# Performance work log

Measured on AMD Instinct MI355X. Metric: run time of the kernel, lower is better.

## Reference

```python
import jax, jax.numpy as jnp
import numpy as np

N, E = 10000, 160000
RNA, PROT, EMB, HID, H = 2000, 100, 128, 128, 4
D_IN = 2 * EMB          # 256, input to last block
D_MID = HID * 4         # 512, after conv1/lin1 residual (heads*channel)


def _gat(x, src, dst, Ws, Wd, att_s, att_d, bias, n_nodes, heads):
    # PyG GATConv (tuple in_channels -> separate src/dst linears, concat=True,
    # add_self_loops=False, negative_slope=0.2, eval mode so dropout is identity)
    C = Ws.shape[1] // heads
    xs = (x @ Ws).reshape(n_nodes, heads, C)   # [N,H,C]
    xd = (x @ Wd).reshape(n_nodes, heads, C)
    a_s = jnp.sum(xs * att_s, axis=-1)          # [N,H]
    a_d = jnp.sum(xd * att_d, axis=-1)
    alpha = jax.nn.leaky_relu(a_s[src] + a_d[dst], 0.2)   # [E,H]
    m = jax.ops.segment_max(alpha, dst, num_segments=n_nodes)  # [N,H]
    alpha = jnp.exp(alpha - m[dst])
    denom = jax.ops.segment_sum(alpha, dst, num_segments=n_nodes)
    alpha = alpha / (denom[dst] + 1e-16)
    out = jax.ops.segment_sum(xs[src] * alpha[:, :, None], dst, num_segments=n_nodes)
    return out.reshape(n_nodes, heads * C) + bias


def _layernorm(h, g, b, eps=1e-5):
    mu = jnp.mean(h, axis=-1, keepdims=True)
    var = jnp.mean(jnp.square(h - mu), axis=-1, keepdims=True)
    return (h - mu) * jax.lax.rsqrt(var + eps) * g + b


def setup_inputs() -> dict:
    key = jax.random.key(0)
    ks = iter(jax.random.split(key, 40))
    w = lambda *s: jax.random.normal(next(ks), s, jnp.float32) * 0.02
    z = lambda *s: jnp.zeros(s, jnp.float32)
    inp = {}
    inp["x"] = jax.random.normal(next(ks), (N, RNA + PROT), jnp.float32)
    inp["edge_index"] = jax.random.randint(next(ks), (2, E), 0, N, jnp.int64)
    inp["W_rna"], inp["b_rna"] = w(RNA, EMB), z(EMB)
    inp["W_prot"], inp["b_prot"] = w(PROT, EMB), z(EMB)
    # last GraphAttnBlock (hidden_dim -> hidden_dim), the only one whose output is used
    inp["c1_Ws"], inp["c1_Wd"] = w(D_IN, H * HID), w(D_IN, H * HID)
    inp["c1_as"], inp["c1_ad"] = w(H, HID), w(H, HID)
    inp["c1_b"] = z(H * HID)
    inp["l1_W"], inp["l1_b"] = w(D_IN, D_MID), z(D_MID)
    inp["ln_g"], inp["ln_b"] = jnp.ones((D_MID,), jnp.float32), z(D_MID)
    inp["c2_Ws"], inp["c2_Wd"] = w(D_MID, H * HID), w(D_MID, H * HID)
    inp["c2_as"], inp["c2_ad"] = w(H, HID), w(H, HID)
    inp["c2_b"] = z(H * HID)
    inp["l2_W"], inp["l2_b"] = w(D_MID, D_MID), z(D_MID)
    inp["agg_W"], inp["agg_b"] = w(D_MID, HID), z(HID)
    inp["dr_W"], inp["dr_b"] = w(HID, EMB), z(EMB)
    inp["dp_W"], inp["dp_b"] = w(HID, EMB), z(EMB)
    inp["rr_W"], inp["rr_b"] = w(EMB, RNA), z(RNA)
    inp["rp_W"], inp["rp_b"] = w(EMB, PROT), z(PROT)
    return inp


def reference(x, edge_index, W_rna, b_rna, W_prot, b_prot,
              c1_Ws, c1_Wd, c1_as, c1_ad, c1_b, l1_W, l1_b, ln_g, ln_b,
              c2_Ws, c2_Wd, c2_as, c2_ad, c2_b, l2_W, l2_b,
              agg_W, agg_b, dr_W, dr_b, dp_W, dp_b, rr_W, rr_b, rp_W, rp_b):
    src, dst = edge_index[0], edge_index[1]
    rna_e = x[:, :RNA] @ W_rna + b_rna
    prot_e = x[:, RNA:] @ W_prot + b_prot
    xin = jnp.concatenate([rna_e, prot_e], axis=1)   # raw_x_input [N, 2*EMB]
    # source loops blocks over raw_x_input; only last block output survives
    h = _gat(xin, src, dst, c1_Ws, c1_Wd, c1_as, c1_ad, c1_b, N, H) + (xin @ l1_W + l1_b)
    h = jax.nn.relu(_layernorm(h, ln_g, ln_b))
    h = _gat(h, src, dst, c2_Ws, c2_Wd, c2_as, c2_ad, c2_b, N, H) + (h @ l2_W + l2_b)
    emb = jax.nn.relu(h @ agg_W + agg_b)
    rna_recon = (emb @ dr_W + dr_b) @ rr_W + rr_b
    prot_recon = (emb @ dp_W + dp_b) @ rp_W + rp_b
    return (rna_recon, prot_recon, emb)
```

## Files before the change

kernel.cpp:

```cpp
#include <hip/hip_runtime.h>
#include <hip/hip_bf16.h>
#include <stdint.h>
#include <stddef.h>

using bf16  = __hip_bfloat16;
using bf162 = __hip_bfloat162;

typedef __bf16 bvec8 __attribute__((ext_vector_type(8)));
typedef float  fvec4 __attribute__((ext_vector_type(4)));

struct __align__(16) bf16x8 { bf162 a, b, c, d; };

__device__ __forceinline__ void bf8_to_f(const bf16* p, float* o) {
    bf16x8 v = *reinterpret_cast<const bf16x8*>(p);
    o[0] = __bfloat162float(v.a.x); o[1] = __bfloat162float(v.a.y);
    o[2] = __bfloat162float(v.b.x); o[3] = __bfloat162float(v.b.y);
    o[4] = __bfloat162float(v.c.x); o[5] = __bfloat162float(v.c.y);
    o[6] = __bfloat162float(v.d.x); o[7] = __bfloat162float(v.d.y);
}

__device__ __forceinline__ float wred_sum(float v) {
    #pragma unroll
    for (int o = 32; o > 0; o >>= 1) v += __shfl_xor(v, o);
    return v;
}

__device__ __forceinline__ float wred_max(float v) {
    #pragma unroll
    for (int o = 32; o > 0; o >>= 1) v = fmaxf(v, __shfl_xor(v, o));
    return v;
}

__device__ __forceinline__ float lrelu(float x) { return (x > 0.f) ? x : 0.2f * x; }

__device__ __forceinline__ fvec4 mfma16(bvec8 a, bvec8 b, fvec4 c) {
    return __builtin_amdgcn_mfma_f32_16x16x32_bf16(a, b, c, 0, 0, 0);
}

__device__ __forceinline__ bvec8 ldA(const bf16* p) {
    return *reinterpret_cast<const bvec8*>(p);
}
__device__ __forceinline__ bvec8 ldA(const float* p) {
    float4 f0 = *reinterpret_cast<const float4*>(p);
    float4 f1 = *reinterpret_cast<const float4*>(p + 4);
    union { bvec8 v; bf16 h[8]; } u;
    u.h[0] = __float2bfloat16(f0.x); u.h[1] = __float2bfloat16(f0.y);
    u.h[2] = __float2bfloat16(f0.z); u.h[3] = __float2bfloat16(f0.w);
    u.h[4] = __float2bfloat16(f1.x); u.h[5] = __float2bfloat16(f1.y);
    u.h[6] = __float2bfloat16(f1.z); u.h[7] = __float2bfloat16(f1.w);
    return u.v;
}

__global__ void detect_kernel(const int* __restrict__ ei, int E, int* __restrict__ flags) {
    __shared__ int zc;
    if (threadIdx.x == 0) zc = 0;
    __syncthreads();
    int nodd = E / 2; if (nodd > 1024) nodd = 1024;
    for (int i = threadIdx.x; i < nodd; i += blockDim.x)
        if (ei[2 * i + 1] == 0) atomicAdd(&zc, 1);
    __syncthreads();
    if (threadIdx.x == 0) flags[0] = (zc > nodd / 2) ? 1 : 0;
}

__global__ void conv_edges_kernel(const int* __restrict__ ei, int* __restrict__ src32,
                                  int* __restrict__ dst32, int E, int N,
                                  const int* __restrict__ flags) {
    const int e = blockIdx.x * blockDim.x + threadIdx.x;
    if (e >= E) return;
    int s, d;
    if (flags[0]) { s = ei[2 * e]; d = ei[2 * (E + e)]; }
    else          { s = ei[e];     d = ei[E + e]; }
    src32[e] = (s < 0) ? 0 : ((s >= N) ? N - 1 : s);
    dst32[e] = (d < 0) ? 0 : ((d >= N) ? N - 1 : d);
}

__global__ void zero2_kernel(int* __restrict__ p1, int* __restrict__ p2, int n) {
    int i = blockIdx.x * blockDim.x + threadIdx.x;
    if (i < n) { p1[i] = 0; p2[i] = 0; }
}

__global__ void hist_kernel(const int* __restrict__ dst32, int* __restrict__ cnt, int E) {
    int e = blockIdx.x * blockDim.x + threadIdx.x;
    if (e < E) atomicAdd(&cnt[dst32[e]], 1);
}

__global__ __launch_bounds__(1024) void scan_kernel(const int* __restrict__ cnt,
                                                    int* __restrict__ row_ptr, int N) {
    __shared__ int wsum[16];
    __shared__ int carry;
    const int tid = threadIdx.x, lane = tid & 63, wid = tid >> 6;
    if (tid == 0) { carry = 0; row_ptr[0] = 0; }
    __syncthreads();
    for (int base = 0; base < N; base += 1024) {
        int i = base + tid;
        int v = (i < N) ? cnt[i] : 0;
        int s = v;
        #pragma unroll
        for (int o = 1; o < 64; o <<= 1) {
            int t = __shfl_up(s, o);
            if (lane >= o) s += t;
        }
        if (lane == 63) wsum[wid] = s;
        __syncthreads();
        if (wid == 0 && lane < 16) {
            int ws = wsum[lane];
            #pragma unroll
            for (int o = 1; o < 16; o <<= 1) {
                int t = __shfl_up(ws, o);
                if (lane >= o) ws += t;
            }
            wsum[lane] = ws;
        }
        __syncthreads();
        int add = carry + (wid > 0 ? wsum[wid - 1] : 0);
        if (i < N) row_ptr[i + 1] = s + add;
        __syncthreads();
        if (tid == 0) carry += wsum[15];
        __syncthreads();
    }
}

__global__ void fill_csr_kernel(const int* __restrict__ src32, const int* __restrict__ dst32,
                                const int* __restrict__ row_ptr, int* __restrict__ cursor,
                                int* __restrict__ col_src, int E) {
    int e = blockIdx.x * blockDim.x + threadIdx.x;
    if (e >= E) return;
    int d = dst32[e];
    int pos = atomicAdd(&cursor[d], 1);
    col_src[row_ptr[d] + pos] = src32[e];
}

struct TEnt { const float* src; bf16* dst; int K, N, Kp, Np, tstart; };
struct TTab { TEnt e[12]; int n; };

__global__ __launch_bounds__(256) void wconv_t_kernel(TTab tab) {
    __shared__ float tile[32][33];
    const int b = blockIdx.x;
    int wi = 0;
    #pragma unroll 1
    for (int i = 1; i < tab.n; ++i) if (b >= tab.e[i].tstart) wi = i;
    const TEnt w = tab.e[wi];
    const int tidx = b - w.tstart;
    const int ntk = w.Kp >> 5;
    const int tn = tidx / ntk, tk = tidx - tn * ntk;
    const int k0 = tk * 32, n0 = tn * 32;
    const int tx = threadIdx.x & 31, ty = threadIdx.x >> 5;
    #pragma unroll
    for (int j = 0; j < 4; ++j) {
        int k = k0 + ty * 4 + j;
        int n = n0 + tx;
        tile[ty * 4 + j][tx] = (k < w.K && n < w.N) ? w.src[(size_t)k * w.N + n] : 0.f;
    }
    __syncthreads();
    #pragma unroll
    for (int j = 0; j < 4; ++j) {
        int n = n0 + ty * 4 + j;
        int k = k0 + tx;
        w.dst[(size_t)n * w.Kp + k] = __float2bfloat16(tile[tx][ty * 4 + j]);
    }
}

__global__ __launch_bounds__(256) void conv_x_kernel(const float* __restrict__ x,
                                                     bf16* __restrict__ xbf) {
    const int r = blockIdx.x;
    const float* xr = x + (size_t)r * 2100;
    bf16* orow = xbf + (size_t)r * 2128;
    #pragma unroll
    for (int pass = 0; pass < 2; ++pass) {
        int c0 = pass * 2048 + threadIdx.x * 8;
        if (c0 >= 2128) continue;
        union { uint4 u; bf16 h[8]; } ob;
        if (c0 + 8 <= 2100) {
            float4 f0 = *reinterpret_cast<const float4*>(xr + c0);
            float4 f1 = *reinterpret_cast<const float4*>(xr + c0 + 4);
            ob.h[0] = __float2bfloat16(f0.x); ob.h[1] = __float2bfloat16(f0.y);
            ob.h[2] = __float2bfloat16(f0.z); ob.h[3] = __float2bfloat16(f0.w);
            ob.h[4] = __float2bfloat16(f1.x); ob.h[5] = __float2bfloat16(f1.y);
            ob.h[6] = __float2bfloat16(f1.z); ob.h[7] = __float2bfloat16(f1.w);
        } else {
            #pragma unroll
            for (int j = 0; j < 8; ++j) {
                int c = c0 + j;
                ob.h[j] = __float2bfloat16((c < 2100) ? xr[c] : 0.f);
            }
        }
        *reinterpret_cast<uint4*>(orow + c0) = ob.u;
    }
}

__global__ void bias_fuse_kernel(const float* l1_b, const float* c1_b, float* bsum1,
                                 const float* l2_b, const float* c2_b, float* bsum2,
                                 const float* dr_b, const float* dp_b, float* ddb) {
    int i = blockIdx.x * blockDim.x + threadIdx.x;
    if (i < 512)       bsum1[i] = l1_b[i] + c1_b[i];
    else if (i < 1024) bsum2[i - 512] = l2_b[i - 512] + c2_b[i - 512];
    else if (i < 1152) ddb[i - 1024] = dr_b[i - 1024];
    else if (i < 1280) ddb[i - 1024] = dp_b[i - 1152];
}

__global__ __launch_bounds__(64) void logits_bf16_kernel(
    const bf16* __restrict__ X,
    const float* __restrict__ Vs, const float* __restrict__ Vd,
    float* __restrict__ a_s, float* __restrict__ a_d)
{
    const int n = blockIdx.x, lane = threadIdx.x;
    const int c0 = lane * 4;
    union { uint2 u; bf16 h[4]; } ub;
    ub.u = *reinterpret_cast<const uint2*>(X + (size_t)n * 256 + c0);
    const float vv[4] = {__bfloat162float(ub.h[0]), __bfloat162float(ub.h[1]),
                         __bfloat162float(ub.h[2]), __bfloat162float(ub.h[3])};
    float ss0=0,ss1=0,ss2=0,ss3=0, dd0=0,dd1=0,dd2=0,dd3=0;
    #pragma unroll
    for (int j = 0; j < 4; ++j) {
        float4 vs = *reinterpret_cast<const float4*>(Vs + (size_t)(c0 + j) * 4);
        float4 vd = *reinterpret_cast<const float4*>(Vd + (size_t)(c0 + j) * 4);
        ss0 = fmaf(vv[j], vs.x, ss0); ss1 = fmaf(vv[j], vs.y, ss1);
        ss2 = fmaf(vv[j], vs.z, ss2); ss3 = fmaf(vv[j], vs.w, ss3);
        dd0 = fmaf(vv[j], vd.x, dd0); dd1 = fmaf(vv[j], vd.y, dd1);
        dd2 = fmaf(vv[j], vd.z, dd2); dd3 = fmaf(vv[j], vd.w, dd3);
    }
    ss0 = wred_sum(ss0); ss1 = wred_sum(ss1); ss2 = wred_sum(ss2); ss3 = wred_sum(ss3);
    dd0 = wred_sum(dd0); dd1 = wred_sum(dd1); dd2 = wred_sum(dd2); dd3 = wred_sum(dd3);
    if (lane == 0) {
        a_s[n*4+0]=ss0; a_s[n*4+1]=ss1; a_s[n*4+2]=ss2; a_s[n*4+3]=ss3;
        a_d[n*4+0]=dd0; a_d[n*4+1]=dd1; a_d[n*4+2]=dd2; a_d[n*4+3]=dd3;
    }
}

template <int FM, bool RELU, typename AT>
__global__ __launch_bounds__(256) void mfma_gemm_kernel(
    const AT* __restrict__ A, int lda,
    const bf16* __restrict__ Bt, int ldb,
    const float* __restrict__ bias,
    float* __restrict__ Cf, int ldcf,
    bf16* __restrict__ Cb, int ldcb,
    int M, int Nn, int K)
{
    const int tid  = threadIdx.x;
    const int w    = tid >> 6, lane = tid & 63;
    const int wr   = w >> 1,   wc   = w & 1;
    const int m0   = blockIdx.y * (FM * 32) + wr * (FM * 16);
    const int n0   = blockIdx.x * 64 + wc * 32;
    const int lrow = lane & 15;
    const int lk8  = (lane >> 4) * 8;

    const AT* Ap[FM];
    #pragma unroll
    for (int i = 0; i < FM; ++i) {
        int r = m0 + i * 16 + lrow;
        if (r > M - 1) r = M - 1;
        Ap[i] = A + (size_t)r * lda + lk8;
    }
    const bf16* Bp = Bt + (size_t)(n0 + lrow) * ldb + lk8;
    const size_t b16 = (size_t)16 * ldb;

    fvec4 acc[FM][2];
    const fvec4 z = {0.f, 0.f, 0.f, 0.f};
    #pragma unroll
    for (int i = 0; i < FM; ++i) { acc[i][0] = z; acc[i][1] = z; }

    #pragma unroll 2
    for (int k = 0; k < K; k += 32) {
        bvec8 b0 = *reinterpret_cast<const bvec8*>(Bp + k);
        bvec8 b1 = *reinterpret_cast<const bvec8*>(Bp + k + b16);
        #pragma unroll
        for (int i = 0; i < FM; ++i) {
            bvec8 a = ldA(Ap[i] + k);
            acc[i][0] = mfma16(a, b0, acc[i][0]);
            acc[i][1] = mfma16(a, b1, acc[i][1]);
        }
    }

    const int r4 = (lane >> 4) * 4;
    #pragma unroll
    for (int fn = 0; fn < 2; ++fn) {
        const int col = n0 + fn * 16 + lrow;
        if (col >= Nn) continue;
        const float bz = bias ? bias[col] : 0.f;
        #pragma unroll
        for (int fm = 0; fm < FM; ++fm) {
            const int rbase = m0 + fm * 16 + r4;
            #pragma unroll
            for (int r = 0; r < 4; ++r) {
                const int row = rbase + r;
                if (row >= M) continue;
                float v = acc[fm][fn][r] + bz;
                if (RELU) v = fmaxf(v, 0.f);
                if (Cf) Cf[(size_t)row * ldcf + col] = v;
                if (Cb) Cb[(size_t)row * ldcb + col] = __float2bfloat16(v);
            }
        }
    }
}

__global__ __launch_bounds__(256) void mfma_gemm_dual_kernel(
    const bf16* __restrict__ A, int lda,
    const bf16* __restrict__ Bt, int ldb,
    const float* __restrict__ biasU,
    bf16* __restrict__ xs, float* __restrict__ hB,
    int M, int K)
{
    const int tid  = threadIdx.x;
    const int w    = tid >> 6, lane = tid & 63;
    const int wr   = w >> 1,   wc   = w & 1;
    const int m0   = blockIdx.y * 128 + wr * 64;
    const int n0   = blockIdx.x * 128 + wc * 64;
    const int lrow = lane & 15;
    const int lk8  = (lane >> 4) * 8;

    const bf16* Ap[4];
    const bf16* Bp[4];
    #pragma unroll
    for (int i = 0; i < 4; ++i) {
        int r = m0 + i * 16 + lrow;
        if (r > M - 1) r = M - 1;
        Ap[i] = A + (size_t)r * lda + lk8;
        Bp[i] = Bt + (size_t)(n0 + i * 16 + lrow) * ldb + lk8;
    }

    fvec4 acc[4][4];
    const fvec4 z = {0.f, 0.f, 0.f, 0.f};
    #pragma unroll
    for (int i = 0; i < 4; ++i)
        #pragma unroll
        for (int j = 0; j < 4; ++j) acc[i][j] = z;

    #pragma unroll 2
    for (int k = 0; k < K; k += 32) {
        bvec8 a[4], b[4];
        #pragma unroll
        for (int i = 0; i < 4; ++i) a[i] = *reinterpret_cast<const bvec8*>(Ap[i] + k);
        #pragma unroll
        for (int j = 0; j < 4; ++j) b[j] = *reinterpret_cast<const bvec8*>(Bp[j] + k);
        #pragma unroll
        for (int i = 0; i < 4; ++i)
            #pragma unroll
            for (int j = 0; j < 4; ++j)
                acc[i][j] = mfma16(a[i], b[j], acc[i][j]);
    }

    const int r4 = (lane >> 4) * 4;
    #pragma unroll
    for (int fn = 0; fn < 4; ++fn) {
        const int col = n0 + fn * 16 + lrow;
        if (col < 512) {
            #pragma unroll
            for (int fm = 0; fm < 4; ++fm) {
                const int rbase = m0 + fm * 16 + r4;
                #pragma unroll
                for (int r = 0; r < 4; ++r) {
                    const int row = rbase + r;
                    if (row >= M) continue;
                    xs[(size_t)row * 512 + col] = __float2bfloat16(acc[fm][fn][r]);
                }
            }
        } else {
            const int c2 = col - 512;
            const float bz = biasU[c2];
            #pragma unroll
            for (int fm = 0; fm < 4; ++fm) {
                const int rbase = m0 + fm * 16 + r4;
                #pragma unroll
                for (int r = 0; r < 4; ++r) {
                    const int row = rbase + r;
                    if (row >= M) continue;
                    hB[(size_t)row * 512 + c2] = acc[fm][fn][r] + bz;
                }
            }
        }
    }
}

__global__ void make_v2_kernel(const float* __restrict__ Ws, const float* __restrict__ atts,
                               float* __restrict__ Vs,
                               const float* __restrict__ Wd, const float* __restrict__ attd,
                               float* __restrict__ Vd, int K)
{
    int t = blockIdx.x * blockDim.x + threadIdx.x;
    const int half = K * 4;
    if (t >= 2 * half) return;
    const float* W   = (t < half) ? Ws : Wd;
    const float* att = (t < half) ? atts : attd;
    float* V         = (t < half) ? Vs : Vd;
    int tt = (t < half) ? t : t - half;
    int k = tt >> 2, h = tt & 3;
    float s = 0.f;
    const float* wp = W + (size_t)k * 512 + h * 128;
    const float* ap = att + h * 128;
    #pragma unroll 4
    for (int c = 0; c < 128; ++c)
        s = fmaf(wp[c], ap[c], s);
    V[k * 4 + h] = s;
}

__global__ __launch_bounds__(64) void gat_gather_kernel(
    const int* __restrict__ row_ptr, const int* __restrict__ col_src,
    const float* __restrict__ a_s, const float* __restrict__ a_d,
    const bf16* __restrict__ xs, float* __restrict__ hout,
    bf16* __restrict__ hout_bf)
{
    const int d = blockIdx.x, lane = threadIdx.x;
    const int beg = row_ptr[d], end = row_ptr[d + 1];
    const float4 ad = *reinterpret_cast<const float4*>(a_d + (size_t)d * 4);

    float m0=-1e30f, m1=-1e30f, m2=-1e30f, m3=-1e30f;
    for (int i = beg + lane; i < end; i += 64) {
        int s = col_src[i];
        float4 as = *reinterpret_cast<const float4*>(a_s + (size_t)s * 4);
        m0 = fmaxf(m0, lrelu(as.x + ad.x));
        m1 = fmaxf(m1, lrelu(as.y + ad.y));
        m2 = fmaxf(m2, lrelu(as.z + ad.z));
        m3 = fmaxf(m3, lrelu(as.w + ad.w));
    }
    m0 = wred_max(m0); m1 = wred_max(m1); m2 = wred_max(m2); m3 = wred_max(m3);

    float d0=0.f, d1=0.f, d2=0.f, d3=0.f;
    for (int i = beg + lane; i < end; i += 64) {
        int s = col_src[i];
        float4 as = *reinterpret_cast<const float4*>(a_s + (size_t)s * 4);
        d0 += __expf(lrelu(as.x + ad.x) - m0);
        d1 += __expf(lrelu(as.y + ad.y) - m1);
        d2 += __expf(lrelu(as.z + ad.z) - m2);
        d3 += __expf(lrelu(as.w + ad.w) - m3);
    }
    d0 = wred_sum(d0); d1 = wred_sum(d1); d2 = wred_sum(d2); d3 = wred_sum(d3);

    const int h = lane >> 4;
    const float mh   = (h == 0) ? m0 : ((h == 1) ? m1 : ((h == 2) ? m2 : m3));
    const float adh  = (h == 0) ? ad.x : ((h == 1) ? ad.y : ((h == 2) ? ad.z : ad.w));
    const float den  = (h == 0) ? d0 : ((h == 1) ? d1 : ((h == 2) ? d2 : d3));
    const float invd = 1.0f / (den + 1e-16f);
    const int c0 = lane * 8;
    float acc[8] = {0.f,0.f,0.f,0.f,0.f,0.f,0.f,0.f};
    #pragma unroll 2
    for (int i = beg; i < end; ++i) {
        int s = col_src[i];
        float coef = __expf(lrelu(a_s[(size_t)s * 4 + h] + adh) - mh) * invd;
        float xv[8];
        bf8_to_f(xs + (size_t)s * 512 + c0, xv);
        #pragma unroll
        for (int t = 0; t < 8; ++t) acc[t] = fmaf(coef, xv[t], acc[t]);
    }
    float* hp = hout + (size_t)d * 512 + c0;
    if (hout_bf) {
        bf16* hb = hout_bf + (size_t)d * 512 + c0;
        #pragma unroll
        for (int t = 0; t < 8; ++t) {
            float fv = hp[t] + acc[t];
            hp[t] = fv;
            hb[t] = __float2bfloat16(fv);
        }
    } else {
        #pragma unroll
        for (int t = 0; t < 8; ++t) hp[t] += acc[t];
    }
}

__global__ __launch_bounds__(64) void ln_relu_logits_kernel(
    const float* __restrict__ in, const float* __restrict__ g,
    const float* __restrict__ b,
    const float* __restrict__ Vs, const float* __restrict__ Vd,
    bf16* __restrict__ outbf, float* __restrict__ a_s, float* __restrict__ a_d)
{
    const int n = blockIdx.x, lane = threadIdx.x;
    const int c0 = lane * 8;
    const float* ip = in + (size_t)n * 512 + c0;
    float v[8];
    float4 p0 = *reinterpret_cast<const float4*>(ip);
    float4 p1 = *reinterpret_cast<const float4*>(ip + 4);
    v[0]=p0.x; v[1]=p0.y; v[2]=p0.z; v[3]=p0.w; v[4]=p1.x; v[5]=p1.y; v[6]=p1.z; v[7]=p1.w;
    float s = 0.f;
    #pragma unroll
    for (int t = 0; t < 8; ++t) s += v[t];
    s = wred_sum(s);
    const float mu = s * (1.0f / 512.0f);
    float q = 0.f;
    #pragma unroll
    for (int t = 0; t < 8; ++t) { float dlt = v[t] - mu; q = fmaf(dlt, dlt, q); }
    q = wred_sum(q);
    const float sc = rsqrtf(q * (1.0f / 512.0f) + 1e-5f);
    float4 g0 = *reinterpret_cast<const float4*>(g + c0);
    float4 g1 = *reinterpret_cast<const float4*>(g + c0 + 4);
    float4 b0 = *reinterpret_cast<const float4*>(b + c0);
    float4 b1 = *reinterpret_cast<const float4*>(b + c0 + 4);
    const float gv[8] = {g0.x,g0.y,g0.z,g0.w,g1.x,g1.y,g1.z,g1.w};
    const float bv[8] = {b0.x,b0.y,b0.z,b0.w,b1.x,b1.y,b1.z,b1.w};
    float r[8];
    bf16* ob = outbf + (size_t)n * 512 + c0;
    #pragma unroll
    for (int t = 0; t < 8; ++t) {
        r[t] = fmaxf(0.f, fmaf((v[t] - mu) * sc, gv[t], bv[t]));
        ob[t] = __float2bfloat16(r[t]);
    }
    float ss0=0,ss1=0,ss2=0,ss3=0, dd0=0,dd1=0,dd2=0,dd3=0;
    #pragma unroll
    for (int t = 0; t < 8; ++t) {
        float4 vs = *reinterpret_cast<const float4*>(Vs + (size_t)(c0 + t) * 4);
        float4 vd = *reinterpret_cast<const float4*>(Vd + (size_t)(c0 + t) * 4);
        ss0 = fmaf(r[t], vs.x, ss0); ss1 = fmaf(r[t], vs.y, ss1);
        ss2 = fmaf(r[t], vs.z, ss2); ss3 = fmaf(r[t], vs.w, ss3);
        dd0 = fmaf(r[t], vd.x, dd0); dd1 = fmaf(r[t], vd.y, dd1);
        dd2 = fmaf(r[t], vd.z, dd2); dd3 = fmaf(r[t], vd.w, dd3);
    }
    ss0 = wred_sum(ss0); ss1 = wred_sum(ss1); ss2 = wred_sum(ss2); ss3 = wred_sum(ss3);
    dd0 = wred_sum(dd0); dd1 = wred_sum(dd1); dd2 = wred_sum(dd2); dd3 = wred_sum(dd3);
    if (lane == 0) {
        a_s[n*4+0]=ss0; a_s[n*4+1]=ss1; a_s[n*4+2]=ss2; a_s[n*4+3]=ss3;
        a_d[n*4+0]=dd0; a_d[n*4+1]=dd1; a_d[n*4+2]=dd2; a_d[n*4+3]=dd3;
    }
}

extern "C" void kernel_launch(void* const* d_in, const int* in_sizes, int n_in,
                              void* d_out, int out_size, void* d_ws, size_t ws_size,
                              hipStream_t stream)
{
    (void)n_in; (void)out_size; (void)ws_size;
    const float* x   = (const float*)d_in[0];
    const int*   ei  = (const int*)d_in[1];

    const float* W_rna  = (const float*)d_in[2];
    const float* b_rna  = (const float*)d_in[3];
    const float* W_prot = (const float*)d_in[4];
    const float* b_prot = (const float*)d_in[5];
    const float* c1_Ws  = (const float*)d_in[6];
    const float* c1_Wd  = (const float*)d_in[7];
    const float* c1_as  = (const float*)d_in[8];
    const float* c1_ad  = (const float*)d_in[9];
    const float* c1_b   = (const float*)d_in[10];
    const float* l1_W   = (const float*)d_in[11];
    const float* l1_b   = (const float*)d_in[12];
    const float* ln_g   = (const float*)d_in[13];
    const float* ln_b   = (const float*)d_in[14];
    const float* c2_Ws  = (const float*)d_in[15];
    const float* c2_Wd  = (const float*)d_in[16];
    const float* c2_as  = (const float*)d_in[17];
    const float* c2_ad  = (const float*)d_in[18];
    const float* c2_b   = (const float*)d_in[19];
    const float* l2_W   = (const float*)d_in[20];
    const float* l2_b   = (const float*)d_in[21];
    const float* agg_W  = (const float*)d_in[22];
    const float* agg_b  = (const float*)d_in[23];
    const float* dr_W   = (const float*)d_in[24];
    const float* dr_b   = (const float*)d_in[25];
    const float* dp_W   = (const float*)d_in[26];
    const float* dp_b   = (const float*)d_in[27];
    const float* rr_W   = (const float*)d_in[28];
    const float* rr_b   = (const float*)d_in[29];
    const float* rp_W   = (const float*)d_in[30];
    const float* rp_b   = (const float*)d_in[31];

    const int N = in_sizes[0] / 2100;
    const int E = in_sizes[1] / 2;
    const int Mp = ((N + 127) & ~127) + 128;

    char* wsp = (char*)d_ws;
    size_t off = 0;
    auto alloc = [&](size_t bytes) -> void* {
        void* p = wsp + off;
        off += (bytes + 255) & ~(size_t)255;
        return p;
    };
    int*      flags   = (int*)   alloc(16);
    int*      src32   = (int*)   alloc((size_t)E * 4);
    int*      dst32   = (int*)   alloc((size_t)E * 4);
    int*      cnt     = (int*)   alloc((size_t)N * 4);
    int*      cursor  = (int*)   alloc((size_t)N * 4);
    int*      row_ptr = (int*)   alloc((size_t)(N + 1) * 4);
    int*      col_src = (int*)   alloc((size_t)E * 4);
    float*    hB      = (float*) alloc((size_t)N * 512 * 4);
    float*    a_s     = (float*) alloc((size_t)N * 4 * 4);
    float*    a_d     = (float*) alloc((size_t)N * 4 * 4);
    float*    Vs      = (float*) alloc(512 * 4 * 4);
    float*    Vd      = (float*) alloc(512 * 4 * 4);
    float*    bsum1   = (float*) alloc(512 * 4);
    float*    bsum2   = (float*) alloc(512 * 4);
    float*    ddb     = (float*) alloc(256 * 4);
    bf16*     xbf     = (bf16*)  alloc((size_t)Mp * 2128 * 2);
    bf16*     xin_bf  = (bf16*)  alloc((size_t)Mp * 256 * 2);
    bf16*     hA_bf   = (bf16*)  alloc((size_t)Mp * 512 * 2);
    bf16*     hB_bf   = (bf16*)  alloc((size_t)Mp * 512 * 2);
    bf16*     xs      = (bf16*)  alloc((size_t)Mp * 512 * 2);
    bf16*     emb_bf  = (bf16*)  alloc((size_t)Mp * 128 * 2);
    bf16*     trp     = (bf16*)  alloc((size_t)Mp * 256 * 2);
    bf16*     wrna_t  = (bf16*)  alloc((size_t)128 * 2016 * 2);
    bf16*     wprot_t = (bf16*)  alloc((size_t)128 * 128 * 2);
    bf16*     cb1     = (bf16*)  alloc((size_t)1024 * 256 * 2);
    bf16*     cb2     = (bf16*)  alloc((size_t)1024 * 512 * 2);
    bf16*     aggt    = (bf16*)  alloc((size_t)128 * 512 * 2);
    bf16*     ddt     = (bf16*)  alloc((size_t)256 * 128 * 2);
    bf16*     rrt     = (bf16*)  alloc((size_t)2048 * 128 * 2);
    bf16*     rpt     = (bf16*)  alloc((size_t)128 * 128 * 2);

    const dim3 blk64(64, 1, 1);
    const dim3 blk256(256, 1, 1);
    const dim3 gE((E + 255) / 256);
    const dim3 gN((N + 255) / 256);
    const int GY128 = (N + 127) / 128;
    const int GY64  = (N + 63) / 64;
    const int GY32  = (N + 31) / 32;

    float* out0 = (float*)d_out;
    float* out1 = out0 + (size_t)N * 2000;
    float* out2 = out1 + (size_t)N * 100;

    detect_kernel<<<dim3(1), blk256, 0, stream>>>(ei, E, flags);
    conv_edges_kernel<<<gE, blk256, 0, stream>>>(ei, src32, dst32, E, N, flags);
    zero2_kernel<<<gN, blk256, 0, stream>>>(cnt, cursor, N);
    hist_kernel<<<gE, blk256, 0, stream>>>(dst32, cnt, E);
    scan_kernel<<<dim3(1), dim3(1024, 1, 1), 0, stream>>>(cnt, row_ptr, N);
    fill_csr_kernel<<<gE, blk256, 0, stream>>>(src32, dst32, row_ptr, cursor, col_src, E);

    {
        TTab tab{};
        int nt = 0, i = 0;
        auto add = [&](const float* s, bf16* d, int K, int Nn, int Kp, int Np) {
            tab.e[i] = {s, d, K, Nn, Kp, Np, nt};
            nt += (Kp >> 5) * (Np >> 5);
            ++i;
        };
        add(W_rna,  wrna_t,          2000, 128, 2016, 128);
        add(W_prot, wprot_t,          100, 128,  128, 128);
        add(c1_Ws,  cb1,              256, 512,  256, 512);
        add(l1_W,   cb1 + 512 * 256,  256, 512,  256, 512);
        add(c2_Ws,  cb2,              512, 512,  512, 512);
        add(l2_W,   cb2 + 512 * 512,  512, 512,  512, 512);
        add(agg_W,  aggt,             512, 128,  512, 128);
        add(dr_W,   ddt,              128, 128,  128, 128);
        add(dp_W,   ddt + 128 * 128,  128, 128,  128, 128);
        add(rr_W,   rrt,              128, 2000, 128, 2048);
        add(rp_W,   rpt,              128, 100,  128, 128);
        tab.n = i;
        wconv_t_kernel<<<dim3(nt), blk256, 0, stream>>>(tab);
    }
    bias_fuse_kernel<<<dim3(5), blk256, 0, stream>>>(l1_b, c1_b, bsum1,
                                                     l2_b, c2_b, bsum2,
                                                     dr_b, dp_b, ddb);
    make_v2_kernel<<<dim3((2 * 256 * 4 + 255) / 256), blk256, 0, stream>>>(
        c1_Ws, c1_as, Vs, c1_Wd, c1_ad, Vd, 256);

    conv_x_kernel<<<dim3(N), blk256, 0, stream>>>(x, xbf);
    mfma_gemm_kernel<2, false, bf16><<<dim3(2, GY64), blk256, 0, stream>>>(
        xbf, 2128, wrna_t, 2016, b_rna, nullptr, 0, xin_bf, 256, N, 128, 2016);
    mfma_gemm_kernel<1, false, bf16><<<dim3(2, GY32), blk256, 0, stream>>>(
        xbf + 2000, 2128, wprot_t, 128, b_prot, nullptr, 0, xin_bf + 128, 256, N, 128, 128);
    logits_bf16_kernel<<<dim3(N), blk64, 0, stream>>>(xin_bf, Vs, Vd, a_s, a_d);

    mfma_gemm_dual_kernel<<<dim3(8, GY128), blk256, 0, stream>>>(
        xin_bf, 256, cb1, 256, bsum1, xs, hB, N, 256);
    gat_gather_kernel<<<dim3(N), blk64, 0, stream>>>(row_ptr, col_src, a_s, a_d, xs, hB, nullptr);

    make_v2_kernel<<<dim3((2 * 512 * 4 + 255) / 256), blk256, 0, stream>>>(
        c2_Ws, c2_as, Vs, c2_Wd, c2_ad, Vd, 512);
    ln_relu_logits_kernel<<<dim3(N), blk64, 0, stream>>>(
        hB, ln_g, ln_b, Vs, Vd, hA_bf, a_s, a_d);

    mfma_gemm_dual_kernel<<<dim3(8, GY128), blk256, 0, stream>>>(
        hA_bf, 512, cb2, 512, bsum2, xs, hB, N, 512);
    gat_gather_kernel<<<dim3(N), blk64, 0, stream>>>(row_ptr, col_src, a_s, a_d, xs, hB, hB_bf);

    mfma_gemm_kernel<2, true, bf16><<<dim3(2, GY64), blk256, 0, stream>>>(
        hB_bf, 512, aggt, 512, agg_b, out2, 128, emb_bf, 128, N, 128, 512);
    mfma_gemm_kernel<2, false, bf16><<<dim3(4, GY64), blk256, 0, stream>>>(
        emb_bf, 128, ddt, 128, ddb, nullptr, 0, trp, 256, N, 256, 128);
    mfma_gemm_kernel<4, false, bf16><<<dim3(32, GY128), blk256, 0, stream>>>(
        trp, 256, rrt, 128, rr_b, out0, 2000, nullptr, 0, N, 2000, 128);
    mfma_gemm_kernel<2, false, bf16><<<dim3(2, GY64), blk256, 0, stream>>>(
        trp + 128, 256, rpt, 128, rp_b, out1, 100, nullptr, 0, N, 100, 128);
}
```

Baseline: 584.7 us.

## Widen dual GEMM tiles to 128x256 with 512 threads and XCD-aware block remap

The dual GEMM (source projection plus linear residual) now uses 512-thread blocks with 8 waves covering a 128x256 output tile instead of 128x128. It also switches to a 1D grid whose block IDs are remapped so consecutive tiles land on the same XCD, aiming for better L2 reuse of A rows across the four column tiles. The intent is to halve redundant A-operand loads and improve cache locality. The cost is fewer blocks in flight and higher register pressure from 512-thread launch bounds.

```diff
diff --git a/kernel.cpp b/kernel.cpp
--- a/kernel.cpp
+++ b/kernel.cpp
@@ -293,18 +293,24 @@
     }
 }
 
-__global__ __launch_bounds__(256) void mfma_gemm_dual_kernel(
+__global__ __launch_bounds__(512) void mfma_gemm_dual_kernel(
     const bf16* __restrict__ A, int lda,
     const bf16* __restrict__ Bt, int ldb,
     const float* __restrict__ biasU,
     bf16* __restrict__ xs, float* __restrict__ hB,
-    int M, int K)
+    int M, int K, int nwg)
 {
+    const int bid = blockIdx.x;
+    const int q = nwg >> 3, r = nwg & 7;
+    const int xcd = bid & 7, idx = bid >> 3;
+    const int sbid = (xcd < r ? xcd * (q + 1) : r * (q + 1) + (xcd - r) * q) + idx;
+    const int by = sbid >> 2, bx = sbid & 3;
+
     const int tid  = threadIdx.x;
     const int w    = tid >> 6, lane = tid & 63;
-    const int wr   = w >> 1,   wc   = w & 1;
-    const int m0   = blockIdx.y * 128 + wr * 64;
-    const int n0   = blockIdx.x * 128 + wc * 64;
+    const int wr   = w >> 2,   wc   = w & 3;
+    const int m0   = by * 128 + wr * 64;
+    const int n0   = bx * 256 + wc * 64;
     const int lrow = lane & 15;
     const int lk8  = (lane >> 4) * 8;
 
@@ -312,9 +318,9 @@
     const bf16* Bp[4];
     #pragma unroll
     for (int i = 0; i < 4; ++i) {
-        int r = m0 + i * 16 + lrow;
-        if (r > M - 1) r = M - 1;
-        Ap[i] = A + (size_t)r * lda + lk8;
+        int rr = m0 + i * 16 + lrow;
+        if (rr > M - 1) rr = M - 1;
+        Ap[i] = A + (size_t)rr * lda + lk8;
         Bp[i] = Bt + (size_t)(n0 + i * 16 + lrow) * ldb + lk8;
     }
 
@@ -348,10 +354,10 @@
             for (int fm = 0; fm < 4; ++fm) {
                 const int rbase = m0 + fm * 16 + r4;
                 #pragma unroll
-                for (int r = 0; r < 4; ++r) {
-                    const int row = rbase + r;
+                for (int rr = 0; rr < 4; ++rr) {
+                    const int row = rbase + rr;
                     if (row >= M) continue;
-                    xs[(size_t)row * 512 + col] = __float2bfloat16(acc[fm][fn][r]);
+                    xs[(size_t)row * 512 + col] = __float2bfloat16(acc[fm][fn][rr]);
                 }
             }
         } else {
@@ -361,10 +367,10 @@
             for (int fm = 0; fm < 4; ++fm) {
                 const int rbase = m0 + fm * 16 + r4;
                 #pragma unroll
-                for (int r = 0; r < 4; ++r) {
-                    const int row = rbase + r;
+                for (int rr = 0; rr < 4; ++rr) {
+                    const int row = rbase + rr;
                     if (row >= M) continue;
-                    hB[(size_t)row * 512 + c2] = acc[fm][fn][r] + bz;
+                    hB[(size_t)row * 512 + c2] = acc[fm][fn][rr] + bz;
                 }
             }
         }
@@ -593,11 +599,13 @@
 
     const dim3 blk64(64, 1, 1);
     const dim3 blk256(256, 1, 1);
+    const dim3 blk512(512, 1, 1);
     const dim3 gE((E + 255) / 256);
     const dim3 gN((N + 255) / 256);
     const int GY128 = (N + 127) / 128;
     const int GY64  = (N + 63) / 64;
     const int GY32  = (N + 31) / 32;
+    const int NWG_DUAL = GY128 * 4;
 
     float* out0 = (float*)d_out;
     float* out1 = out0 + (size_t)N * 2000;
@@ -645,8 +653,8 @@
         xbf + 2000, 2128, wprot_t, 128, b_prot, nullptr, 0, xin_bf + 128, 256, N, 128, 128);
     logits_bf16_kernel<<<dim3(N), blk64, 0, stream>>>(xin_bf, Vs, Vd, a_s, a_d);
 
-    mfma_gemm_dual_kernel<<<dim3(8, GY128), blk256, 0, stream>>>(
-        xin_bf, 256, cb1, 256, bsum1, xs, hB, N, 256);
+    mfma_gemm_dual_kernel<<<dim3(NWG_DUAL), blk512, 0, stream>>>(
+        xin_bf, 256, cb1, 256, bsum1, xs, hB, N, 256, NWG_DUAL);
     gat_gather_kernel<<<dim3(N), blk64, 0, stream>>>(row_ptr, col_src, a_s, a_d, xs, hB, nullptr);
 
     make_v2_kernel<<<dim3((2 * 512 * 4 + 255) / 256), blk256, 0, stream>>>(
@@ -654,8 +662,8 @@
     ln_relu_logits_kernel<<<dim3(N), blk64, 0, stream>>>(
         hB, ln_g, ln_b, Vs, Vd, hA_bf, a_s, a_d);
 
-    mfma_gemm_dual_kernel<<<dim3(8, GY128), blk256, 0, stream>>>(
-        hA_bf, 512, cb2, 512, bsum2, xs, hB, N, 512);
+    mfma_gemm_dual_kernel<<<dim3(NWG_DUAL), blk512, 0, stream>>>(
+        hA_bf, 512, cb2, 512, bsum2, xs, hB, N, 512, NWG_DUAL);
     gat_gather_kernel<<<dim3(N), blk64, 0, stream>>>(row_ptr, col_src, a_s, a_d, xs, hB, hB_bf);
 
     mfma_gemm_kernel<2, true, bf16><<<dim3(2, GY64), blk256, 0, stream>>>(
```

Measured after the change: 605.1 us. +3.5%, slower.
